# Kernel tuning notes

Hardware: AMD Instinct MI355X
Metric: run time of the kernel (lower is better)

Reference implementation:

```python
import math
import jax, jax.numpy as jnp
import numpy as np


def _unskew(X):
    # X: B x M x (M+L)  ->  B x M x L (each row i shifted left by i)
    B, M, MpL = X.shape
    L = MpL - M
    X = X.reshape(B, M * MpL)
    X = jnp.pad(X, ((0, 0), (0, M)))          # B x (M*(M+L)+M)
    X = X.reshape(B, M, MpL + 1)               # B x M x (M+L+1)
    return X[:, :, :L]


def _skew(X, pad_value):
    # X: B x M x L  ->  B x M x (M+L) (each row i shifted right by i)
    B, M, L = X.shape
    X = jnp.pad(X, ((0, 0), (0, 0), (0, M + 1)), constant_values=pad_value)
    X = X.reshape(B, -1)[:, :-M]               # B x (M*(M+L))
    return X.reshape(B, M, M + L)


def setup_inputs() -> dict:
    key = jax.random.key(0)
    k1, k2, k3, k4 = jax.random.split(key, 4)
    B, M, L, H = 128, 512, 1024, 64   # B = batch*heads, key len = M+L
    query = jax.random.normal(k1, (B, M, H), dtype=jnp.float32)
    key_t = jax.random.normal(k2, (B, M + L, H), dtype=jnp.float32)
    value = jax.random.normal(k3, (B, M + L, H), dtype=jnp.float32)
    key_pe = jax.random.normal(k4, (1, H, L), dtype=jnp.float32) * 0.02
    return {"query": query, "key": key_t, "value": value, "key_pe": key_pe}


def reference(query, key, value, key_pe):
    H = query.shape[-1]  # head_dim
    # content attention: B x M x (M+L), then unskew to relative coords B x M x L
    attn_cont = jnp.einsum('bmh,bnh->bmn', query, key)
    attn_cont = _unskew(attn_cont)
    # position attention: B x M x L (key_pe broadcasts over batch)
    attn_pos = jnp.einsum('bmh,xhl->bml', query, key_pe)
    attn = (attn_cont + attn_pos) / math.sqrt(H)
    attn = jax.nn.softmax(attn, axis=-1)
    # dropout p=0.0 -> identity
    attn_sk = _skew(attn, 0.0)                  # B x M x (M+L)
    out = jnp.einsum('bmn,bnh->bmh', attn_sk, value)
    return out
```

## Files before the change

### kernel.cpp

```cpp
#include <hip/hip_runtime.h>
#include <math.h>

typedef __bf16 bf16x8 __attribute__((ext_vector_type(8)));
typedef __bf16 bf16x4 __attribute__((ext_vector_type(4)));
typedef float  f32x4  __attribute__((ext_vector_type(4)));

constexpr int B_  = 128;
constexpr int M_  = 512;
constexpr int L_  = 1024;
constexpr int H_  = 64;
constexpr int KL_ = 1536;

constexpr int BM = 64;
constexpr int KT = 64;
constexpr int NT = 17;
constexpr int KS = 72;
constexpr int PPS = 128;
constexpr int PSS = 40;

constexpr int OFF_KS   = 0;
constexpr int OFF_VT   = 9216;
constexpr int OFF_PET  = 18432;
constexpr int OFF_PPOS = 27648;
constexpr int OFF_PS   = 44032;
constexpr int SMEM_BYTES = 54272;
constexpr int OFF_OBUF = 0;
constexpr int OFF_LSUM = 18432;
constexpr int OBS = 36;

#define MFMA16(A, B, C) __builtin_amdgcn_mfma_f32_16x16x32_bf16((A), (B), (C), 0, 0, 0)

__global__ __launch_bounds__(256, 3)
void seqattn_v3(const float* __restrict__ Q, const float* __restrict__ K,
                const float* __restrict__ V, const float* __restrict__ PE,
                float* __restrict__ O) {
  __shared__ alignas(16) char smem[SMEM_BYTES];
  __bf16* ks   = (__bf16*)(smem + OFF_KS);
  __bf16* vt   = (__bf16*)(smem + OFF_VT);
  __bf16* pet  = (__bf16*)(smem + OFF_PET);
  __bf16* ppos = (__bf16*)(smem + OFF_PPOS);

  const int tid  = threadIdx.x;
  const int w    = tid >> 6;
  const int lane = tid & 63;
  const int nid  = lane & 15;
  const int qid  = lane >> 4;
  const int a    = w >> 1;
  const int c    = w & 1;
  const int b    = blockIdx.x;
  const int m0   = blockIdx.y * BM;

  __bf16* ps = (__bf16*)(smem + OFF_PS) + w * 32 * PSS;

  bf16x8 aq[2][2];
  #pragma unroll
  for (int it = 0; it < 2; ++it) {
    const float* qg = &Q[((size_t)b * M_ + m0 + 32 * a + 16 * it + nid) * H_];
    #pragma unroll
    for (int j = 0; j < 8; ++j) {
      aq[it][0][j] = (__bf16)qg[8 * qid + j];
      aq[it][1][j] = (__bf16)qg[32 + 8 * qid + j];
    }
  }

  f32x4 o[2][4];
  #pragma unroll
  for (int it = 0; it < 2; ++it)
    #pragma unroll
    for (int ht = 0; ht < 4; ++ht) o[it][ht] = (f32x4){0.f, 0.f, 0.f, 0.f};
  float lpart[2][4];
  #pragma unroll
  for (int it = 0; it < 2; ++it)
    #pragma unroll
    for (int r = 0; r < 4; ++r) lpart[it][r] = 0.f;

  const int krow = tid >> 2,  khq = (tid & 3) * 16;
  const int vj = (tid & 15) * 4, vh = (tid >> 4) * 4;
  const int ph = (tid & 15) * 4, pl = (tid >> 4) * 4;

  for (int t = 0; t < NT; ++t) {
    const int j0 = m0 + KT * t;

    __syncthreads();

    {
      const float* kg = &K[((size_t)b * KL_ + j0 + krow) * H_ + khq];
      f32x4 f0 = *(const f32x4*)kg,     f1 = *(const f32x4*)(kg + 4);
      f32x4 f2 = *(const f32x4*)(kg + 8), f3 = *(const f32x4*)(kg + 12);
      bf16x8 x0, x1;
      #pragma unroll
      for (int j = 0; j < 4; ++j) {
        x0[j] = (__bf16)f0[j]; x0[4 + j] = (__bf16)f1[j];
        x1[j] = (__bf16)f2[j]; x1[4 + j] = (__bf16)f3[j];
      }
      *(bf16x8*)&ks[krow * KS + khq] = x0;
      *(bf16x8*)&ks[krow * KS + khq + 8] = x1;
    }
    {
      const float* vg = &V[((size_t)b * KL_ + j0 + vj) * H_ + vh];
      f32x4 r0 = *(const f32x4*)vg;
      f32x4 r1 = *(const f32x4*)(vg + H_);
      f32x4 r2 = *(const f32x4*)(vg + 2 * H_);
      f32x4 r3 = *(const f32x4*)(vg + 3 * H_);
      #pragma unroll
      for (int e = 0; e < 4; ++e) {
        bf16x4 y = {(__bf16)r0[e], (__bf16)r1[e], (__bf16)r2[e], (__bf16)r3[e]};
        *(bf16x4*)&vt[(vh + e) * KS + vj] = y;
      }
    }
    if (t < 16) {
      const float* pg = &PE[(size_t)ph * L_ + KT * t + pl];
      f32x4 e0 = *(const f32x4*)pg;
      f32x4 e1 = *(const f32x4*)(pg + L_);
      f32x4 e2 = *(const f32x4*)(pg + 2 * L_);
      f32x4 e3 = *(const f32x4*)(pg + 3 * L_);
      #pragma unroll
      for (int r = 0; r < 4; ++r) {
        bf16x4 y = {(__bf16)e0[r], (__bf16)e1[r], (__bf16)e2[r], (__bf16)e3[r]};
        *(bf16x4*)&pet[(pl + r) * KS + ph] = y;
      }
    }
    __syncthreads();

    const f32x4 z = {0.f, 0.f, 0.f, 0.f};

    f32x4 s[2][2];
    #pragma unroll
    for (int nt = 0; nt < 2; ++nt) {
      const __bf16* kb = &ks[(32 * c + 16 * nt + nid) * KS];
      const bf16x8 b0 = *(const bf16x8*)&kb[8 * qid];
      const bf16x8 b1 = *(const bf16x8*)&kb[32 + 8 * qid];
      #pragma unroll
      for (int it = 0; it < 2; ++it) {
        s[it][nt] = MFMA16(aq[it][0], b0, z);
        s[it][nt] = MFMA16(aq[it][1], b1, s[it][nt]);
      }
    }

    if (t < 16) {
      #pragma unroll
      for (int nt = 0; nt < 2; ++nt) {
        const __bf16* pb = &pet[(32 * c + 16 * nt + nid) * KS];
        const bf16x8 b0 = *(const bf16x8*)&pb[8 * qid];
        const bf16x8 b1 = *(const bf16x8*)&pb[32 + 8 * qid];
        const int col = (64 * t + 32 * c + 16 * nt + nid) & 127;
        #pragma unroll
        for (int it = 0; it < 2; ++it) {
          f32x4 pp = MFMA16(aq[it][0], b0, z);
          pp = MFMA16(aq[it][1], b1, pp);
          #pragma unroll
          for (int r = 0; r < 4; ++r) {
            const int row = 32 * a + 16 * it + 4 * qid + r;
            ppos[row * PPS + (col ^ ((row & 3) << 3))] = (__bf16)pp[r];
          }
        }
      }
    }
    __syncthreads();

    const bool edge = (t == 0) || (t == 16);
    #pragma unroll
    for (int it = 0; it < 2; ++it) {
      #pragma unroll
      for (int nt = 0; nt < 2; ++nt) {
        #pragma unroll
        for (int r = 0; r < 4; ++r) {
          const int il = 32 * a + 16 * it + 4 * qid + r;
          const int l  = 64 * t + 32 * c + 16 * nt + nid - il;
          float p;
          if (!edge || (unsigned)l < 1024u) {
            const float pe = (float)ppos[il * PPS + ((l & 127) ^ ((il & 3) << 3))];
            p = __expf((s[it][nt][r] + pe) * 0.125f);
          } else {
            p = 0.f;
          }
          lpart[it][r] += p;
          ps[(16 * it + 4 * qid + r) * PSS + 16 * nt + nid] = (__bf16)p;
        }
      }
    }

    #pragma unroll
    for (int it = 0; it < 2; ++it) {
      const bf16x8 ap = *(const bf16x8*)&ps[(16 * it + nid) * PSS + 8 * qid];
      #pragma unroll
      for (int ht = 0; ht < 4; ++ht) {
        o[it][ht] = MFMA16(ap, *(const bf16x8*)&vt[(16 * ht + nid) * KS + 32 * c + 8 * qid],
                           o[it][ht]);
      }
    }
  }

  __syncthreads();
  float* lsum = (float*)(smem + OFF_LSUM);
  float* obuf = (float*)(smem + OFF_OBUF);

  #pragma unroll
  for (int it = 0; it < 2; ++it) {
    #pragma unroll
    for (int r = 0; r < 4; ++r) {
      float v = lpart[it][r];
      v += __shfl_xor(v, 1); v += __shfl_xor(v, 2);
      v += __shfl_xor(v, 4); v += __shfl_xor(v, 8);
      lpart[it][r] = v;
    }
  }
  if (nid == 0) {
    #pragma unroll
    for (int it = 0; it < 2; ++it)
      #pragma unroll
      for (int r = 0; r < 4; ++r)
        lsum[c * 64 + 32 * a + 16 * it + 4 * qid + r] = lpart[it][r];
  }
  if (c == 1) {
    #pragma unroll
    for (int it = 0; it < 2; ++it)
      #pragma unroll
      for (int ht = 0; ht < 4; ++ht)
        *(f32x4*)&obuf[(a * 64 + 16 * ht + nid) * OBS + 16 * it + 4 * qid] = o[it][ht];
  }
  __syncthreads();
  if (c == 0) {
    float inv[2][4];
    #pragma unroll
    for (int it = 0; it < 2; ++it)
      #pragma unroll
      for (int r = 0; r < 4; ++r) {
        const int row = 32 * a + 16 * it + 4 * qid + r;
        inv[it][r] = 1.f / (lsum[row] + lsum[64 + row]);
      }
    #pragma unroll
    for (int it = 0; it < 2; ++it) {
      #pragma unroll
      for (int ht = 0; ht < 4; ++ht) {
        f32x4 oo = o[it][ht] +
                   *(const f32x4*)&obuf[(a * 64 + 16 * ht + nid) * OBS + 16 * it + 4 * qid];
        #pragma unroll
        for (int r = 0; r < 4; ++r) {
          const int row = 32 * a + 16 * it + 4 * qid + r;
          O[((size_t)b * M_ + m0 + row) * H_ + 16 * ht + nid] = oo[r] * inv[it][r];
        }
      }
    }
  }
}

extern "C" void kernel_launch(void* const* d_in, const int* in_sizes, int n_in,
                              void* d_out, int out_size, void* d_ws, size_t ws_size,
                              hipStream_t stream) {
  const float* Q  = (const float*)d_in[0];
  const float* K  = (const float*)d_in[1];
  const float* V  = (const float*)d_in[2];
  const float* PE = (const float*)d_in[3];
  float* O = (float*)d_out;

  dim3 grid(B_, M_ / BM);
  dim3 block(256);
  hipLaunchKernelGGL(seqattn_v3, grid, block, 0, stream, Q, K, V, PE, O);
}
```

Before: 231.6 us.

## Double-buffer K/V tiles with register prefetch and compute position scores one tile ahead

K and V tiles are now double-buffered in shared memory, and the next tile is prefetched into registers while the current tile is computed, which cuts the per-tile barriers from three to one. Position-embedding B-fragments are loaded straight from global into registers instead of being staged in shared memory, and the position scores for the next chunk go into a wider 4-chunk ring buffer so they can be written ahead of use. This removes load latency and barrier stalls from the main loop. In exchange, shared memory grows to about 78KB, occupancy drops from 3 to 2 blocks per CU, and register pressure rises.

```diff
diff --git a/kernel.cpp b/kernel.cpp
--- a/kernel.cpp
+++ b/kernel.cpp
@@ -15,29 +15,27 @@
 constexpr int KT = 64;
 constexpr int NT = 17;
 constexpr int KS = 72;
-constexpr int PPS = 128;
+constexpr int PPS = 256;
 constexpr int PSS = 40;
 
 constexpr int OFF_KS   = 0;
-constexpr int OFF_VT   = 9216;
-constexpr int OFF_PET  = 18432;
-constexpr int OFF_PPOS = 27648;
-constexpr int OFF_PS   = 44032;
-constexpr int SMEM_BYTES = 54272;
+constexpr int OFF_VT   = 18432;
+constexpr int OFF_PPOS = 36864;
+constexpr int OFF_PS   = 69632;
+constexpr int SMEM_BYTES = 79872;
 constexpr int OFF_OBUF = 0;
 constexpr int OFF_LSUM = 18432;
 constexpr int OBS = 36;
 
 #define MFMA16(A, B, C) __builtin_amdgcn_mfma_f32_16x16x32_bf16((A), (B), (C), 0, 0, 0)
 
-__global__ __launch_bounds__(256, 3)
-void seqattn_v3(const float* __restrict__ Q, const float* __restrict__ K,
+__global__ __launch_bounds__(256, 2)
+void seqattn_v5(const float* __restrict__ Q, const float* __restrict__ K,
                 const float* __restrict__ V, const float* __restrict__ PE,
                 float* __restrict__ O) {
   __shared__ alignas(16) char smem[SMEM_BYTES];
-  __bf16* ks   = (__bf16*)(smem + OFF_KS);
-  __bf16* vt   = (__bf16*)(smem + OFF_VT);
-  __bf16* pet  = (__bf16*)(smem + OFF_PET);
+  __bf16* ksb  = (__bf16*)(smem + OFF_KS);
+  __bf16* vtb  = (__bf16*)(smem + OFF_VT);
   __bf16* ppos = (__bf16*)(smem + OFF_PPOS);
 
   const int tid  = threadIdx.x;
@@ -49,6 +47,7 @@
   const int c    = w & 1;
   const int b    = blockIdx.x;
   const int m0   = blockIdx.y * BM;
+  const int swz  = qid << 4;
 
   __bf16* ps = (__bf16*)(smem + OFF_PS) + w * 32 * PSS;
 
@@ -64,70 +63,99 @@
   }
 
   f32x4 o[2][4];
-  #pragma unroll
-  for (int it = 0; it < 2; ++it)
-    #pragma unroll
-    for (int ht = 0; ht < 4; ++ht) o[it][ht] = (f32x4){0.f, 0.f, 0.f, 0.f};
   float lpart[2][4];
   #pragma unroll
-  for (int it = 0; it < 2; ++it)
+  for (int it = 0; it < 2; ++it) {
+    #pragma unroll
+    for (int ht = 0; ht < 4; ++ht) o[it][ht] = (f32x4){0.f, 0.f, 0.f, 0.f};
     #pragma unroll
     for (int r = 0; r < 4; ++r) lpart[it][r] = 0.f;
+  }
 
   const int krow = tid >> 2,  khq = (tid & 3) * 16;
   const int vj = (tid & 15) * 4, vh = (tid >> 4) * 4;
-  const int ph = (tid & 15) * 4, pl = (tid >> 4) * 4;
+
+  const float* peg = &PE[(size_t)(8 * qid) * L_ + 32 * c + nid];
+
+  f32x4 kr[4], vr[4];
+  {
+    const float* kg = &K[((size_t)b * KL_ + m0 + krow) * H_ + khq];
+    kr[0] = *(const f32x4*)kg;       kr[1] = *(const f32x4*)(kg + 4);
+    kr[2] = *(const f32x4*)(kg + 8); kr[3] = *(const f32x4*)(kg + 12);
+    const float* vg = &V[((size_t)b * KL_ + m0 + vj) * H_ + vh];
+    #pragma unroll
+    for (int e = 0; e < 4; ++e) vr[e] = *(const f32x4*)(vg + e * H_);
+  }
+  {
+    const f32x4 z = {0.f, 0.f, 0.f, 0.f};
+    #pragma unroll
+    for (int nt = 0; nt < 2; ++nt) {
+      bf16x8 b0, b1;
+      #pragma unroll
+      for (int j = 0; j < 8; ++j) {
+        b0[j] = (__bf16)peg[(size_t)j * L_ + 16 * nt];
+        b1[j] = (__bf16)peg[(size_t)(32 + j) * L_ + 16 * nt];
+      }
+      const int colb = 32 * c + 16 * nt + nid;
+      #pragma unroll
+      for (int it = 0; it < 2; ++it) {
+        f32x4 pp = MFMA16(aq[it][0], b0, z);
+        pp = MFMA16(aq[it][1], b1, pp);
+        #pragma unroll
+        for (int r = 0; r < 4; ++r)
+          ppos[(32 * a + 16 * it + 4 * qid + r) * PPS + (colb ^ swz)] = (__bf16)pp[r];
+      }
+    }
+  }
+  {
+    bf16x8 x0, x1;
+    #pragma unroll
+    for (int j = 0; j < 4; ++j) {
+      x0[j] = (__bf16)kr[0][j]; x0[4 + j] = (__bf16)kr[1][j];
+      x1[j] = (__bf16)kr[2][j]; x1[4 + j] = (__bf16)kr[3][j];
+    }
+    *(bf16x8*)&ksb[krow * KS + khq] = x0;
+    *(bf16x8*)&ksb[krow * KS + khq + 8] = x1;
+    #pragma unroll
+    for (int e = 0; e < 4; ++e) {
+      bf16x4 y = {(__bf16)vr[0][e], (__bf16)vr[1][e], (__bf16)vr[2][e], (__bf16)vr[3][e]};
+      *(bf16x4*)&vtb[(vh + e) * KS + vj] = y;
+    }
+  }
+  __syncthreads();
 
   for (int t = 0; t < NT; ++t) {
-    const int j0 = m0 + KT * t;
-
-    __syncthreads();
-
-    {
-      const float* kg = &K[((size_t)b * KL_ + j0 + krow) * H_ + khq];
-      f32x4 f0 = *(const f32x4*)kg,     f1 = *(const f32x4*)(kg + 4);
-      f32x4 f2 = *(const f32x4*)(kg + 8), f3 = *(const f32x4*)(kg + 12);
-      bf16x8 x0, x1;
-      #pragma unroll
-      for (int j = 0; j < 4; ++j) {
-        x0[j] = (__bf16)f0[j]; x0[4 + j] = (__bf16)f1[j];
-        x1[j] = (__bf16)f2[j]; x1[4 + j] = (__bf16)f3[j];
-      }
-      *(bf16x8*)&ks[krow * KS + khq] = x0;
-      *(bf16x8*)&ks[krow * KS + khq + 8] = x1;
-    }
-    {
-      const float* vg = &V[((size_t)b * KL_ + j0 + vj) * H_ + vh];
-      f32x4 r0 = *(const f32x4*)vg;
-      f32x4 r1 = *(const f32x4*)(vg + H_);
-      f32x4 r2 = *(const f32x4*)(vg + 2 * H_);
-      f32x4 r3 = *(const f32x4*)(vg + 3 * H_);
-      #pragma unroll
-      for (int e = 0; e < 4; ++e) {
-        bf16x4 y = {(__bf16)r0[e], (__bf16)r1[e], (__bf16)r2[e], (__bf16)r3[e]};
-        *(bf16x4*)&vt[(vh + e) * KS + vj] = y;
-      }
-    }
     if (t < 16) {
-      const float* pg = &PE[(size_t)ph * L_ + KT * t + pl];
-      f32x4 e0 = *(const f32x4*)pg;
-      f32x4 e1 = *(const f32x4*)(pg + L_);
-      f32x4 e2 = *(const f32x4*)(pg + 2 * L_);
-      f32x4 e3 = *(const f32x4*)(pg + 3 * L_);
-      #pragma unroll
-      for (int r = 0; r < 4; ++r) {
-        bf16x4 y = {(__bf16)e0[r], (__bf16)e1[r], (__bf16)e2[r], (__bf16)e3[r]};
-        *(bf16x4*)&pet[(pl + r) * KS + ph] = y;
-      }
-    }
-    __syncthreads();
-
+      const int j1 = m0 + KT * (t + 1);
+      const float* kg = &K[((size_t)b * KL_ + j1 + krow) * H_ + khq];
+      kr[0] = *(const f32x4*)kg;       kr[1] = *(const f32x4*)(kg + 4);
+      kr[2] = *(const f32x4*)(kg + 8); kr[3] = *(const f32x4*)(kg + 12);
+      const float* vg = &V[((size_t)b * KL_ + j1 + vj) * H_ + vh];
+      #pragma unroll
+      for (int e = 0; e < 4; ++e) vr[e] = *(const f32x4*)(vg + e * H_);
+    }
+    bf16x8 pf[2][2];
+    const int ch = t + 1;
+    if (t < 15) {
+      const float* pc = peg + ch * 64;
+      #pragma unroll
+      for (int nt = 0; nt < 2; ++nt) {
+        #pragma unroll
+        for (int j = 0; j < 8; ++j) {
+          pf[nt][0][j] = (__bf16)pc[(size_t)j * L_ + 16 * nt];
+          pf[nt][1][j] = (__bf16)pc[(size_t)(32 + j) * L_ + 16 * nt];
+        }
+      }
+    }
+
+    const __bf16* kst = ksb + (t & 1) * 64 * KS;
+    const __bf16* vtt = vtb + (t & 1) * 64 * KS;
     const f32x4 z = {0.f, 0.f, 0.f, 0.f};
 
     f32x4 s[2][2];
     #pragma unroll
     for (int nt = 0; nt < 2; ++nt) {
-      const __bf16* kb = &ks[(32 * c + 16 * nt + nid) * KS];
+      const __bf16* kb = &kst[(32 * c + 16 * nt + nid) * KS];
       const bf16x8 b0 = *(const bf16x8*)&kb[8 * qid];
       const bf16x8 b1 = *(const bf16x8*)&kb[32 + 8 * qid];
       #pragma unroll
@@ -137,39 +165,34 @@
       }
     }
 
-    if (t < 16) {
+    if (t < 15) {
       #pragma unroll
       for (int nt = 0; nt < 2; ++nt) {
-        const __bf16* pb = &pet[(32 * c + 16 * nt + nid) * KS];
-        const bf16x8 b0 = *(const bf16x8*)&pb[8 * qid];
-        const bf16x8 b1 = *(const bf16x8*)&pb[32 + 8 * qid];
-        const int col = (64 * t + 32 * c + 16 * nt + nid) & 127;
+        const int colb = ((ch & 3) << 6) + 32 * c + 16 * nt + nid;
         #pragma unroll
         for (int it = 0; it < 2; ++it) {
-          f32x4 pp = MFMA16(aq[it][0], b0, z);
-          pp = MFMA16(aq[it][1], b1, pp);
+          f32x4 pp = MFMA16(aq[it][0], pf[nt][0], z);
+          pp = MFMA16(aq[it][1], pf[nt][1], pp);
           #pragma unroll
-          for (int r = 0; r < 4; ++r) {
-            const int row = 32 * a + 16 * it + 4 * qid + r;
-            ppos[row * PPS + (col ^ ((row & 3) << 3))] = (__bf16)pp[r];
-          }
+          for (int r = 0; r < 4; ++r)
+            ppos[(32 * a + 16 * it + 4 * qid + r) * PPS + (colb ^ swz)] = (__bf16)pp[r];
         }
       }
     }
-    __syncthreads();
 
     const bool edge = (t == 0) || (t == 16);
     #pragma unroll
     for (int it = 0; it < 2; ++it) {
       #pragma unroll
-      for (int nt = 0; nt < 2; ++nt) {
-        #pragma unroll
-        for (int r = 0; r < 4; ++r) {
-          const int il = 32 * a + 16 * it + 4 * qid + r;
-          const int l  = 64 * t + 32 * c + 16 * nt + nid - il;
+      for (int r = 0; r < 4; ++r) {
+        const int il = 32 * a + 16 * it + 4 * qid + r;
+        const int rb = il * PPS;
+        #pragma unroll
+        for (int nt = 0; nt < 2; ++nt) {
+          const int l = KT * t + 32 * c + 16 * nt + nid - il;
           float p;
           if (!edge || (unsigned)l < 1024u) {
-            const float pe = (float)ppos[il * PPS + ((l & 127) ^ ((il & 3) << 3))];
+            const float pe = (float)ppos[rb + ((l & 255) ^ swz)];
             p = __expf((s[it][nt][r] + pe) * 0.125f);
           } else {
             p = 0.f;
@@ -185,13 +208,31 @@
       const bf16x8 ap = *(const bf16x8*)&ps[(16 * it + nid) * PSS + 8 * qid];
       #pragma unroll
       for (int ht = 0; ht < 4; ++ht) {
-        o[it][ht] = MFMA16(ap, *(const bf16x8*)&vt[(16 * ht + nid) * KS + 32 * c + 8 * qid],
+        o[it][ht] = MFMA16(ap, *(const bf16x8*)&vtt[(16 * ht + nid) * KS + 32 * c + 8 * qid],
                            o[it][ht]);
       }
     }
-  }
-
-  __syncthreads();
+
+    if (t < 16) {
+      __bf16* ksn = ksb + ((t + 1) & 1) * 64 * KS;
+      __bf16* vtn = vtb + ((t + 1) & 1) * 64 * KS;
+      bf16x8 x0, x1;
+      #pragma unroll
+      for (int j = 0; j < 4; ++j) {
+        x0[j] = (__bf16)kr[0][j]; x0[4 + j] = (__bf16)kr[1][j];
+        x1[j] = (__bf16)kr[2][j]; x1[4 + j] = (__bf16)kr[3][j];
+      }
+      *(bf16x8*)&ksn[krow * KS + khq] = x0;
+      *(bf16x8*)&ksn[krow * KS + khq + 8] = x1;
+      #pragma unroll
+      for (int e = 0; e < 4; ++e) {
+        bf16x4 y = {(__bf16)vr[0][e], (__bf16)vr[1][e], (__bf16)vr[2][e], (__bf16)vr[3][e]};
+        *(bf16x4*)&vtn[(vh + e) * KS + vj] = y;
+      }
+    }
+    __syncthreads();
+  }
+
   float* lsum = (float*)(smem + OFF_LSUM);
   float* obuf = (float*)(smem + OFF_OBUF);
 
@@ -255,6 +296,5 @@
   float* O = (float*)d_out;
 
   dim3 grid(B_, M_ / BM);
-  dim3 block(256);
-  hipLaunchKernelGGL(seqattn_v3, grid, block, 0, stream, Q, K, V, PE, O);
+  hipLaunchKernelGGL(seqattn_v5, grid, dim3(256), 0, stream, Q, K, V, PE, O);
 }
```

Result: faster. 222.4 us (-4.0%).
